# Performance work log

Measured on AMD Instinct MI355X. Metric: run time of the kernel, lower is better.

## Reference

```python
import jax, jax.numpy as jnp
import numpy as np

B, N_IN, N_MF, N_RULES, N_OUT_MEM, N_OUT = 16384, 6, 5, 2048, 12, 2
TANH_CENTERS = np.array([0.0, 0.75], dtype=np.float32)
TANH_SCALE = np.array([4.0, 0.75], dtype=np.float32)
EPS = 1e-12


def setup_inputs() -> dict:
    key = jax.random.key(0)
    k = jax.random.split(key, 6)
    x = jax.random.normal(k[0], (B, N_IN), dtype=jnp.float32)
    mf_centers = jax.random.normal(k[1], (N_IN, N_MF), dtype=jnp.float32)
    # strictly positive widths for the Gaussian memberships
    mf_scales = jax.random.uniform(k[2], (N_IN, N_MF), dtype=jnp.float32) + 0.5
    out_centers = jax.random.normal(k[3], (N_OUT_MEM,), dtype=jnp.float32)
    input_rules = jax.random.randint(k[4], (N_RULES, N_IN), 0, N_IN * N_MF, dtype=jnp.int32)
    output_rules = jax.random.randint(k[5], (N_RULES, N_OUT), 0, N_OUT_MEM, dtype=jnp.int32)
    return {"x": x, "mf_centers": mf_centers, "mf_scales": mf_scales,
            "out_centers": out_centers, "input_rules": input_rules,
            "output_rules": output_rules}


def reference(x, mf_centers, mf_scales, out_centers, input_rules, output_rules):
    # fuzzify: Gaussian membership per (input var, MF) -> [B, N_IN*N_MF]
    z = (x[:, :, None] - mf_centers[None]) / mf_scales[None]      # [B, N_IN, N_MF]
    fuzzified = jnp.exp(-z * z).reshape(x.shape[0], -1)           # [B, 30]
    # rules: gather antecedent memberships, min t-norm over antecedents
    gathered = fuzzified[:, input_rules]                          # [B, R, N_IN]
    weights = jnp.min(gathered, axis=2)                           # [B, R]
    # L1 normalize across rules (F.normalize p=1, dim=1)
    l1 = jnp.sum(jnp.abs(weights), axis=1, keepdims=True)
    normalized = weights / jnp.maximum(l1, EPS)
    # defuzzify: gather output-membership centers per rule, then matmul
    ow = out_centers[output_rules]                                # [R, N_OUT]
    defuzz = normalized @ ow                                      # [B, N_OUT]
    # constrain scaling
    return jnp.tanh(defuzz) * jnp.asarray(TANH_SCALE) + jnp.asarray(TANH_CENTERS)
```

## Files before the change

kernel.cpp:

```cpp
#include <hip/hip_runtime.h>
#include <hip/hip_bf16.h>

#define BATCH      16384
#define N_IN       6
#define N_MF       5
#define N_FUZZ     30
#define N_RULES    2048
#define N_OUT_MEM  12

#define ROWS_PB    256
#define SPLITS     4
#define RULES_PB   (N_RULES / SPLITS)
#define THREADS    1024
#define WAVES      16
#define RULES_PW   (RULES_PB / WAVES)
#define ROWGROUPS  (BATCH / ROWS_PB)

#define WS_PACKED_OFF  0
#define WS_OW_OFF      8192
#define WS_PART_OFF    24576

typedef _Float16 f16x2 __attribute__((ext_vector_type(2)));

__device__ inline int probe_is_bf16(const void* mfs) {
    const unsigned int* w = (const unsigned int*)mfs;
    int ok = 1;
    for (int k = 0; k < 15; ++k) {
        const unsigned int v = w[k];
        const float lo = __uint_as_float(v << 16);
        const float hi = __uint_as_float(v & 0xffff0000u);
        if (!(lo >= 0.4f && lo <= 1.6f && hi >= 0.4f && hi <= 1.6f)) { ok = 0; break; }
    }
    return ok;
}

__global__ void anfis_prep(const int* __restrict__ input_rules,
                           const int* __restrict__ output_rules,
                           const void* __restrict__ oc_,
                           const void* __restrict__ mfs_,
                           unsigned int* __restrict__ packed,
                           float2* __restrict__ ow) {
    __shared__ int flag;
    if (threadIdx.x == 0) flag = probe_is_bf16(mfs_);
    __syncthreads();
    const bool is_bf16 = (flag != 0);

    const int r = blockIdx.x * blockDim.x + threadIdx.x;
    if (r >= N_RULES) return;
    const int* rp = input_rules + r * N_IN;
    unsigned int p = 0;
#pragma unroll
    for (int i = 0; i < N_IN; ++i) p |= ((unsigned int)rp[i] & 31u) << (5 * i);
    packed[r] = p;

    const int o0i = output_rules[2 * r + 0];
    const int o1i = output_rules[2 * r + 1];
    float o0, o1;
    if (is_bf16) {
        const unsigned short* oc = (const unsigned short*)oc_;
        o0 = __uint_as_float((unsigned int)oc[o0i] << 16);
        o1 = __uint_as_float((unsigned int)oc[o1i] << 16);
    } else {
        const float* oc = (const float*)oc_;
        o0 = oc[o0i]; o1 = oc[o1i];
    }
    ow[r] = make_float2(o0, o1);
}

__global__ __launch_bounds__(THREADS, 4)
void anfis_main(const void* __restrict__ x_,
                const void* __restrict__ mfc_,
                const void* __restrict__ mfs_,
                const unsigned int* __restrict__ packed,
                const float2* __restrict__ ow,
                float* __restrict__ partials) {
    __shared__ float xs[ROWS_PB * N_IN];
    __shared__ float2 cinv[N_FUZZ];
    __shared__ uint2 fuzz4[N_FUZZ][64];
    __shared__ float pl1[WAVES][ROWS_PB];
    __shared__ float pd0[WAVES][ROWS_PB];
    __shared__ float pd1[WAVES][ROWS_PB];
    __shared__ int flag;

    const int t     = threadIdx.x;
    const int g     = blockIdx.x >> 2;
    const int split = blockIdx.x & 3;
    const int row0  = g * ROWS_PB;

    if (t == 0) flag = probe_is_bf16(mfs_);
    __syncthreads();
    const bool is_bf16 = (flag != 0);

    if (is_bf16) {
        const unsigned short* xp = (const unsigned short*)x_ + row0 * N_IN;
        for (int i = t; i < ROWS_PB * N_IN; i += THREADS)
            xs[i] = __uint_as_float((unsigned int)xp[i] << 16);
    } else {
        const float* xp = (const float*)x_ + row0 * N_IN;
        for (int i = t; i < ROWS_PB * N_IN; i += THREADS) xs[i] = xp[i];
    }
    if (t < N_FUZZ) {
        float c, s;
        if (is_bf16) {
            c = __uint_as_float((unsigned int)((const unsigned short*)mfc_)[t] << 16);
            s = __uint_as_float((unsigned int)((const unsigned short*)mfs_)[t] << 16);
        } else {
            c = ((const float*)mfc_)[t];
            s = ((const float*)mfs_)[t];
        }
        cinv[t] = make_float2(c, 1.0f / s);
    }
    __syncthreads();

    for (int e = t; e < N_FUZZ * 64; e += THREADS) {
        const int v    = e >> 6;
        const int lane = e & 63;
        const int i    = v / N_MF;
        const float2 ci = cinv[v];
        float f[4];
#pragma unroll
        for (int k = 0; k < 4; ++k) {
            const float z = (xs[(lane + 64 * k) * N_IN + i] - ci.x) * ci.y;
            f[k] = __expf(-z * z);
        }
        f16x2 a = { (_Float16)f[0], (_Float16)f[1] };
        f16x2 b = { (_Float16)f[2], (_Float16)f[3] };
        uint2 u;
        u.x = __builtin_bit_cast(unsigned int, a);
        u.y = __builtin_bit_cast(unsigned int, b);
        fuzz4[v][lane] = u;
    }
    __syncthreads();

    const int lane = t & 63;
    const int wave = __builtin_amdgcn_readfirstlane(t >> 6);
    const uint2* fz = &fuzz4[0][0];

    float l1[4] = {0.f, 0.f, 0.f, 0.f};
    float d0[4] = {0.f, 0.f, 0.f, 0.f};
    float d1[4] = {0.f, 0.f, 0.f, 0.f};

    const int rbase = split * RULES_PB + wave * RULES_PW;
#pragma unroll 4
    for (int j = 0; j < RULES_PW; ++j) {
        const int r = rbase + j;
        const unsigned int p = packed[r];
        const float2 o = ow[r];
        const uint2 g0 = fz[((p      ) & 31u) * 64 + lane];
        const uint2 g1 = fz[((p >> 5 ) & 31u) * 64 + lane];
        const uint2 g2 = fz[((p >> 10) & 31u) * 64 + lane];
        const uint2 g3 = fz[((p >> 15) & 31u) * 64 + lane];
        const uint2 g4 = fz[((p >> 20) & 31u) * 64 + lane];
        const uint2 g5 = fz[((p >> 25) & 31u) * 64 + lane];
        f16x2 wa = __builtin_elementwise_min(__builtin_bit_cast(f16x2, g0.x),
                                             __builtin_bit_cast(f16x2, g1.x));
        wa = __builtin_elementwise_min(wa, __builtin_bit_cast(f16x2, g2.x));
        wa = __builtin_elementwise_min(wa, __builtin_bit_cast(f16x2, g3.x));
        wa = __builtin_elementwise_min(wa, __builtin_bit_cast(f16x2, g4.x));
        wa = __builtin_elementwise_min(wa, __builtin_bit_cast(f16x2, g5.x));
        f16x2 wb = __builtin_elementwise_min(__builtin_bit_cast(f16x2, g0.y),
                                             __builtin_bit_cast(f16x2, g1.y));
        wb = __builtin_elementwise_min(wb, __builtin_bit_cast(f16x2, g2.y));
        wb = __builtin_elementwise_min(wb, __builtin_bit_cast(f16x2, g3.y));
        wb = __builtin_elementwise_min(wb, __builtin_bit_cast(f16x2, g4.y));
        wb = __builtin_elementwise_min(wb, __builtin_bit_cast(f16x2, g5.y));
        const float w0 = (float)wa.x, w1 = (float)wa.y;
        const float w2 = (float)wb.x, w3 = (float)wb.y;
        l1[0] += w0; d0[0] += w0 * o.x; d1[0] += w0 * o.y;
        l1[1] += w1; d0[1] += w1 * o.x; d1[1] += w1 * o.y;
        l1[2] += w2; d0[2] += w2 * o.x; d1[2] += w2 * o.y;
        l1[3] += w3; d0[3] += w3 * o.x; d1[3] += w3 * o.y;
    }
#pragma unroll
    for (int k = 0; k < 4; ++k) {
        pl1[wave][lane + 64 * k] = l1[k];
        pd0[wave][lane + 64 * k] = d0[k];
        pd1[wave][lane + 64 * k] = d1[k];
    }
    __syncthreads();

    if (t < ROWS_PB) {
        float a = 0.f, b = 0.f, c = 0.f;
#pragma unroll
        for (int wv = 0; wv < WAVES; ++wv) {
            a += pl1[wv][t];
            b += pd0[wv][t];
            c += pd1[wv][t];
        }
        const int row = row0 + t;
        partials[(split * 3 + 0) * BATCH + row] = a;
        partials[(split * 3 + 1) * BATCH + row] = b;
        partials[(split * 3 + 2) * BATCH + row] = c;
    }
}

__global__ void anfis_finalize(const float* __restrict__ partials,
                               const void* __restrict__ mfs_,
                               void* __restrict__ out_) {
    __shared__ int flag;
    if (threadIdx.x == 0) flag = probe_is_bf16(mfs_);
    __syncthreads();
    const int row = blockIdx.x * blockDim.x + threadIdx.x;
    if (row >= BATCH) return;
    float l1 = 0.f, d0 = 0.f, d1 = 0.f;
#pragma unroll
    for (int s = 0; s < SPLITS; ++s) {
        l1 += partials[(s * 3 + 0) * BATCH + row];
        d0 += partials[(s * 3 + 1) * BATCH + row];
        d1 += partials[(s * 3 + 2) * BATCH + row];
    }
    const float inv = 1.0f / fmaxf(l1, 1e-12f);
    const float y0 = tanhf(d0 * inv) * 4.00f + 0.00f;
    const float y1 = tanhf(d1 * inv) * 0.75f + 0.75f;
    if (flag) {
        __hip_bfloat162 o;
        o.x = __float2bfloat16(y0);
        o.y = __float2bfloat16(y1);
        ((__hip_bfloat162*)out_)[row] = o;
    } else {
        ((float2*)out_)[row] = make_float2(y0, y1);
    }
}

extern "C" void kernel_launch(void* const* d_in, const int* in_sizes, int n_in,
                              void* d_out, int out_size, void* d_ws, size_t ws_size,
                              hipStream_t stream) {
    (void)in_sizes; (void)n_in; (void)out_size; (void)ws_size;
    const void* x_   = d_in[0];
    const void* mfc_ = d_in[1];
    const void* mfs_ = d_in[2];
    const void* oc_  = d_in[3];
    const int* input_rules  = (const int*)d_in[4];
    const int* output_rules = (const int*)d_in[5];

    unsigned int* packed = (unsigned int*)((char*)d_ws + WS_PACKED_OFF);
    float2*       ow     = (float2*)((char*)d_ws + WS_OW_OFF);
    float*        parts  = (float*)((char*)d_ws + WS_PART_OFF);

    anfis_prep<<<(N_RULES + 255) / 256, 256, 0, stream>>>(
        input_rules, output_rules, oc_, mfs_, packed, ow);

    anfis_main<<<ROWGROUPS * SPLITS, THREADS, 0, stream>>>(
        x_, mfc_, mfs_, packed, ow, parts);

    anfis_finalize<<<BATCH / 256, 256, 0, stream>>>(parts, mfs_, d_out);
}
```

Before: 80.61 us.

## Fuse prep, main and finalize into one cooperative kernel with grid sync

Replaces the three-kernel pipeline (rule packing, main reduction, finalize) with a single cooperative kernel. Rule indices and output centers are now read directly from global memory inside the rule loop, and a grid-wide sync sits between the partial-sum write and the finalize step. The aim is to remove two launch gaps and the packed-rule prep pass. The cost is a grid barrier, more scalar/global loads per rule in the inner loop, and a launch that requires all 256 blocks of 1024 threads to be co-resident. If the cooperative launch fails, it falls back to the old path.

Result: slower. 120.8 us (+49.8%).

```diff
diff --git a/kernel.cpp b/kernel.cpp
--- a/kernel.cpp
+++ b/kernel.cpp
@@ -1,5 +1,8 @@
 #include <hip/hip_runtime.h>
 #include <hip/hip_bf16.h>
+#include <hip/hip_cooperative_groups.h>
+
+namespace cg = cooperative_groups;
 
 #define BATCH      16384
 #define N_IN       6
@@ -15,6 +18,7 @@
 #define WAVES      16
 #define RULES_PW   (RULES_PB / WAVES)
 #define ROWGROUPS  (BATCH / ROWS_PB)
+#define FIN_ROWS   (BATCH / (ROWGROUPS * SPLITS))
 
 #define WS_PACKED_OFF  0
 #define WS_OW_OFF      8192
@@ -32,6 +36,173 @@
         if (!(lo >= 0.4f && lo <= 1.6f && hi >= 0.4f && hi <= 1.6f)) { ok = 0; break; }
     }
     return ok;
+}
+
+__global__ __launch_bounds__(THREADS, 4)
+void anfis_fused(const void* __restrict__ x_,
+                 const void* __restrict__ mfc_,
+                 const void* __restrict__ mfs_,
+                 const void* __restrict__ oc_,
+                 const int* __restrict__ input_rules,
+                 const int* __restrict__ output_rules,
+                 float* __restrict__ partials,
+                 void* __restrict__ out_) {
+    __shared__ float xs[ROWS_PB * N_IN];
+    __shared__ float2 cinv[N_FUZZ];
+    __shared__ uint2 fuzz4[N_FUZZ][64];
+    __shared__ float pl1[WAVES][ROWS_PB];
+    __shared__ float pd0[WAVES][ROWS_PB];
+    __shared__ float pd1[WAVES][ROWS_PB];
+    __shared__ int flag;
+
+    const int t     = threadIdx.x;
+    const int g     = blockIdx.x >> 2;
+    const int split = blockIdx.x & 3;
+    const int row0  = g * ROWS_PB;
+
+    if (t == 0) flag = probe_is_bf16(mfs_);
+    __syncthreads();
+    const int is_bf16 = __builtin_amdgcn_readfirstlane(flag);
+
+    if (is_bf16) {
+        const unsigned short* xp = (const unsigned short*)x_ + row0 * N_IN;
+        for (int i = t; i < ROWS_PB * N_IN; i += THREADS)
+            xs[i] = __uint_as_float((unsigned int)xp[i] << 16);
+    } else {
+        const float* xp = (const float*)x_ + row0 * N_IN;
+        for (int i = t; i < ROWS_PB * N_IN; i += THREADS) xs[i] = xp[i];
+    }
+    if (t < N_FUZZ) {
+        float c, s;
+        if (is_bf16) {
+            c = __uint_as_float((unsigned int)((const unsigned short*)mfc_)[t] << 16);
+            s = __uint_as_float((unsigned int)((const unsigned short*)mfs_)[t] << 16);
+        } else {
+            c = ((const float*)mfc_)[t];
+            s = ((const float*)mfs_)[t];
+        }
+        cinv[t] = make_float2(c, 1.0f / s);
+    }
+    __syncthreads();
+
+    for (int e = t; e < N_FUZZ * 64; e += THREADS) {
+        const int v    = e >> 6;
+        const int lane = e & 63;
+        const int i    = v / N_MF;
+        const float2 ci = cinv[v];
+        float f[4];
+#pragma unroll
+        for (int k = 0; k < 4; ++k) {
+            const float z = (xs[(lane + 64 * k) * N_IN + i] - ci.x) * ci.y;
+            f[k] = __expf(-z * z);
+        }
+        f16x2 a = { (_Float16)f[0], (_Float16)f[1] };
+        f16x2 b = { (_Float16)f[2], (_Float16)f[3] };
+        uint2 u;
+        u.x = __builtin_bit_cast(unsigned int, a);
+        u.y = __builtin_bit_cast(unsigned int, b);
+        fuzz4[v][lane] = u;
+    }
+    __syncthreads();
+
+    const int lane = t & 63;
+    const int wave = __builtin_amdgcn_readfirstlane(t >> 6);
+    const uint2* fz = &fuzz4[0][0];
+    const char* ocb = (const char*)oc_;
+    const unsigned sh = is_bf16 ? 1u : 2u;
+
+    float l1[4] = {0.f, 0.f, 0.f, 0.f};
+    float d0[4] = {0.f, 0.f, 0.f, 0.f};
+    float d1[4] = {0.f, 0.f, 0.f, 0.f};
+
+    const int rbase = split * RULES_PB + wave * RULES_PW;
+#pragma unroll 4
+    for (int j = 0; j < RULES_PW; ++j) {
+        const int r = rbase + j;
+        const int* rp = input_rules + r * N_IN;
+        const int i0 = rp[0], i1 = rp[1], i2 = rp[2];
+        const int i3 = rp[3], i4 = rp[4], i5 = rp[5];
+        const int o0i = output_rules[2 * r + 0];
+        const int o1i = output_rules[2 * r + 1];
+        const unsigned b0 = ((unsigned)o0i) << sh;
+        const unsigned b1 = ((unsigned)o1i) << sh;
+        const unsigned w0_ = *(const unsigned*)(ocb + (b0 & ~3u));
+        const unsigned w1_ = *(const unsigned*)(ocb + (b1 & ~3u));
+        const unsigned v0 = is_bf16 ? ((b0 & 2u) ? (w0_ & 0xffff0000u) : (w0_ << 16)) : w0_;
+        const unsigned v1 = is_bf16 ? ((b1 & 2u) ? (w1_ & 0xffff0000u) : (w1_ << 16)) : w1_;
+        const float ox = __uint_as_float(v0);
+        const float oy = __uint_as_float(v1);
+
+        const uint2 g0 = fz[i0 * 64 + lane];
+        const uint2 g1 = fz[i1 * 64 + lane];
+        const uint2 g2 = fz[i2 * 64 + lane];
+        const uint2 g3 = fz[i3 * 64 + lane];
+        const uint2 g4 = fz[i4 * 64 + lane];
+        const uint2 g5 = fz[i5 * 64 + lane];
+        f16x2 wa = __builtin_elementwise_min(__builtin_bit_cast(f16x2, g0.x),
+                                             __builtin_bit_cast(f16x2, g1.x));
+        wa = __builtin_elementwise_min(wa, __builtin_bit_cast(f16x2, g2.x));
+        wa = __builtin_elementwise_min(wa, __builtin_bit_cast(f16x2, g3.x));
+        wa = __builtin_elementwise_min(wa, __builtin_bit_cast(f16x2, g4.x));
+        wa = __builtin_elementwise_min(wa, __builtin_bit_cast(f16x2, g5.x));
+        f16x2 wb = __builtin_elementwise_min(__builtin_bit_cast(f16x2, g0.y),
+                                             __builtin_bit_cast(f16x2, g1.y));
+        wb = __builtin_elementwise_min(wb, __builtin_bit_cast(f16x2, g2.y));
+        wb = __builtin_elementwise_min(wb, __builtin_bit_cast(f16x2, g3.y));
+        wb = __builtin_elementwise_min(wb, __builtin_bit_cast(f16x2, g4.y));
+        wb = __builtin_elementwise_min(wb, __builtin_bit_cast(f16x2, g5.y));
+        const float w0 = (float)wa.x, w1 = (float)wa.y;
+        const float w2 = (float)wb.x, w3 = (float)wb.y;
+        l1[0] += w0; d0[0] += w0 * ox; d1[0] += w0 * oy;
+        l1[1] += w1; d0[1] += w1 * ox; d1[1] += w1 * oy;
+        l1[2] += w2; d0[2] += w2 * ox; d1[2] += w2 * oy;
+        l1[3] += w3; d0[3] += w3 * ox; d1[3] += w3 * oy;
+    }
+#pragma unroll
+    for (int k = 0; k < 4; ++k) {
+        pl1[wave][lane + 64 * k] = l1[k];
+        pd0[wave][lane + 64 * k] = d0[k];
+        pd1[wave][lane + 64 * k] = d1[k];
+    }
+    __syncthreads();
+
+    if (t < ROWS_PB) {
+        float a = 0.f, b = 0.f, c = 0.f;
+#pragma unroll
+        for (int wv = 0; wv < WAVES; ++wv) {
+            a += pl1[wv][t];
+            b += pd0[wv][t];
+            c += pd1[wv][t];
+        }
+        const int row = row0 + t;
+        partials[(split * 3 + 0) * BATCH + row] = a;
+        partials[(split * 3 + 1) * BATCH + row] = b;
+        partials[(split * 3 + 2) * BATCH + row] = c;
+    }
+
+    cg::this_grid().sync();
+
+    if (t < FIN_ROWS) {
+        const int row = blockIdx.x * FIN_ROWS + t;
+        float a = 0.f, b = 0.f, c = 0.f;
+#pragma unroll
+        for (int s = 0; s < SPLITS; ++s) {
+            a += partials[(s * 3 + 0) * BATCH + row];
+            b += partials[(s * 3 + 1) * BATCH + row];
+            c += partials[(s * 3 + 2) * BATCH + row];
+        }
+        const float inv = 1.0f / fmaxf(a, 1e-12f);
+        const float y0 = tanhf(b * inv) * 4.00f + 0.00f;
+        const float y1 = tanhf(c * inv) * 0.75f + 0.75f;
+        if (is_bf16) {
+            __hip_bfloat162 o;
+            o.x = __float2bfloat16(y0);
+            o.y = __float2bfloat16(y1);
+            ((__hip_bfloat162*)out_)[row] = o;
+        } else {
+            ((float2*)out_)[row] = make_float2(y0, y1);
+        }
+    }
 }
 
 __global__ void anfis_prep(const int* __restrict__ input_rules,
@@ -233,15 +404,23 @@
     const int* input_rules  = (const int*)d_in[4];
     const int* output_rules = (const int*)d_in[5];
 
-    unsigned int* packed = (unsigned int*)((char*)d_ws + WS_PACKED_OFF);
-    float2*       ow     = (float2*)((char*)d_ws + WS_OW_OFF);
-    float*        parts  = (float*)((char*)d_ws + WS_PART_OFF);
-
-    anfis_prep<<<(N_RULES + 255) / 256, 256, 0, stream>>>(
-        input_rules, output_rules, oc_, mfs_, packed, ow);
-
-    anfis_main<<<ROWGROUPS * SPLITS, THREADS, 0, stream>>>(
-        x_, mfc_, mfs_, packed, ow, parts);
-
-    anfis_finalize<<<BATCH / 256, 256, 0, stream>>>(parts, mfs_, d_out);
-}
+    float* parts = (float*)((char*)d_ws + WS_PART_OFF);
+    void*  out_  = d_out;
+
+    void* args[] = { (void*)&x_, (void*)&mfc_, (void*)&mfs_, (void*)&oc_,
+                     (void*)&input_rules, (void*)&output_rules,
+                     (void*)&parts, (void*)&out_ };
+    hipError_t err = hipLaunchCooperativeKernel(
+        (const void*)anfis_fused, dim3(ROWGROUPS * SPLITS), dim3(THREADS),
+        args, 0, stream);
+
+    if (err != hipSuccess) {
+        unsigned int* packed = (unsigned int*)((char*)d_ws + WS_PACKED_OFF);
+        float2*       ow     = (float2*)((char*)d_ws + WS_OW_OFF);
+        anfis_prep<<<(N_RULES + 255) / 256, 256, 0, stream>>>(
+            input_rules, output_rules, oc_, mfs_, packed, ow);
+        anfis_main<<<ROWGROUPS * SPLITS, THREADS, 0, stream>>>(
+            x_, mfc_, mfs_, packed, ow, parts);
+        anfis_finalize<<<BATCH / 256, 256, 0, stream>>>(parts, mfs_, d_out);
+    }
+}
```

## Fuse finalize into main kernel via atomic accumulation and last-block reduction

Applied to the files above, without the earlier changes.

Removes the separate finalize kernel launch. Each split block now atomically adds its per-row partial sums into a shared accumulator, and the last block of each row group, found with a counter and threadfence, applies the normalization and tanh and writes the output. The prep kernel now zeroes the accumulator and the counters. This saves one launch and the partials round trip, at the cost of global atomics and a reduction order that is no longer deterministic.

Result: slower. 137.7 us (+70.8%).

```diff
diff --git a/kernel.cpp b/kernel.cpp
--- a/kernel.cpp
+++ b/kernel.cpp
@@ -18,7 +18,8 @@
 
 #define WS_PACKED_OFF  0
 #define WS_OW_OFF      8192
-#define WS_PART_OFF    24576
+#define WS_ACC_OFF     24576
+#define WS_CNT_OFF     221184
 
 typedef _Float16 f16x2 __attribute__((ext_vector_type(2)));
 
@@ -39,13 +40,19 @@
                            const void* __restrict__ oc_,
                            const void* __restrict__ mfs_,
                            unsigned int* __restrict__ packed,
-                           float2* __restrict__ ow) {
+                           float2* __restrict__ ow,
+                           float* __restrict__ acc,
+                           int* __restrict__ cnt) {
     __shared__ int flag;
     if (threadIdx.x == 0) flag = probe_is_bf16(mfs_);
     __syncthreads();
     const bool is_bf16 = (flag != 0);
 
     const int r = blockIdx.x * blockDim.x + threadIdx.x;
+
+    for (int i = r; i < 3 * BATCH; i += N_RULES) acc[i] = 0.0f;
+    if (r < ROWGROUPS) cnt[r] = 0;
+
     if (r >= N_RULES) return;
     const int* rp = input_rules + r * N_IN;
     unsigned int p = 0;
@@ -73,7 +80,9 @@
                 const void* __restrict__ mfs_,
                 const unsigned int* __restrict__ packed,
                 const float2* __restrict__ ow,
-                float* __restrict__ partials) {
+                float* __restrict__ acc,
+                int* __restrict__ cnt,
+                void* __restrict__ out_) {
     __shared__ float xs[ROWS_PB * N_IN];
     __shared__ float2 cinv[N_FUZZ];
     __shared__ uint2 fuzz4[N_FUZZ][64];
@@ -81,6 +90,7 @@
     __shared__ float pd0[WAVES][ROWS_PB];
     __shared__ float pd1[WAVES][ROWS_PB];
     __shared__ int flag;
+    __shared__ int lastBlk;
 
     const int t     = threadIdx.x;
     const int g     = blockIdx.x >> 2;
@@ -188,37 +198,32 @@
             c += pd1[wv][t];
         }
         const int row = row0 + t;
-        partials[(split * 3 + 0) * BATCH + row] = a;
-        partials[(split * 3 + 1) * BATCH + row] = b;
-        partials[(split * 3 + 2) * BATCH + row] = c;
-    }
-}
-
-__global__ void anfis_finalize(const float* __restrict__ partials,
-                               const void* __restrict__ mfs_,
-                               void* __restrict__ out_) {
-    __shared__ int flag;
-    if (threadIdx.x == 0) flag = probe_is_bf16(mfs_);
-    __syncthreads();
-    const int row = blockIdx.x * blockDim.x + threadIdx.x;
-    if (row >= BATCH) return;
-    float l1 = 0.f, d0 = 0.f, d1 = 0.f;
-#pragma unroll
-    for (int s = 0; s < SPLITS; ++s) {
-        l1 += partials[(s * 3 + 0) * BATCH + row];
-        d0 += partials[(s * 3 + 1) * BATCH + row];
-        d1 += partials[(s * 3 + 2) * BATCH + row];
-    }
-    const float inv = 1.0f / fmaxf(l1, 1e-12f);
-    const float y0 = tanhf(d0 * inv) * 4.00f + 0.00f;
-    const float y1 = tanhf(d1 * inv) * 0.75f + 0.75f;
-    if (flag) {
-        __hip_bfloat162 o;
-        o.x = __float2bfloat16(y0);
-        o.y = __float2bfloat16(y1);
-        ((__hip_bfloat162*)out_)[row] = o;
-    } else {
-        ((float2*)out_)[row] = make_float2(y0, y1);
+        atomicAdd(&acc[0 * BATCH + row], a);
+        atomicAdd(&acc[1 * BATCH + row], b);
+        atomicAdd(&acc[2 * BATCH + row], c);
+    }
+
+    __threadfence();
+    __syncthreads();
+    if (t == 0) lastBlk = (atomicAdd(&cnt[g], 1) == SPLITS - 1);
+    __syncthreads();
+
+    if (lastBlk && t < ROWS_PB) {
+        const int row = row0 + t;
+        const float a = atomicAdd(&acc[0 * BATCH + row], 0.0f);
+        const float b = atomicAdd(&acc[1 * BATCH + row], 0.0f);
+        const float c = atomicAdd(&acc[2 * BATCH + row], 0.0f);
+        const float inv = 1.0f / fmaxf(a, 1e-12f);
+        const float y0 = tanhf(b * inv) * 4.00f + 0.00f;
+        const float y1 = tanhf(c * inv) * 0.75f + 0.75f;
+        if (is_bf16) {
+            __hip_bfloat162 o;
+            o.x = __float2bfloat16(y0);
+            o.y = __float2bfloat16(y1);
+            ((__hip_bfloat162*)out_)[row] = o;
+        } else {
+            ((float2*)out_)[row] = make_float2(y0, y1);
+        }
     }
 }
 
@@ -235,13 +240,12 @@
 
     unsigned int* packed = (unsigned int*)((char*)d_ws + WS_PACKED_OFF);
     float2*       ow     = (float2*)((char*)d_ws + WS_OW_OFF);
-    float*        parts  = (float*)((char*)d_ws + WS_PART_OFF);
+    float*        acc    = (float*)((char*)d_ws + WS_ACC_OFF);
+    int*          cnt    = (int*)((char*)d_ws + WS_CNT_OFF);
 
     anfis_prep<<<(N_RULES + 255) / 256, 256, 0, stream>>>(
-        input_rules, output_rules, oc_, mfs_, packed, ow);
+        input_rules, output_rules, oc_, mfs_, packed, ow, acc, cnt);
 
     anfis_main<<<ROWGROUPS * SPLITS, THREADS, 0, stream>>>(
-        x_, mfc_, mfs_, packed, ow, parts);
-
-    anfis_finalize<<<BATCH / 256, 256, 0, stream>>>(parts, mfs_, d_out);
-}
+        x_, mfc_, mfs_, packed, ow, acc, cnt, d_out);
+}
```
